# Optimization experiments

Hardware: AMD Instinct MI355X
Metric: run time of the kernel (lower is better)

The kernel has to match this reference:

```python
import jax, jax.numpy as jnp
import numpy as np

ALPHA = 1.5      # entmax alpha (q parameter)
N_ITER = 50      # entmax-bisect iterations (entmax library default)
B, S, DM, H, HKV, HD = 1, 2048, 2048, 16, 4, 128
ROPE_THETA = 10000.0


def _entmax_p(x):
    """alpha-entmax along last axis via bisection on tau (matches entmax.EntmaxBisect)."""
    am1 = ALPHA - 1.0
    pw = 1.0 / am1
    X = x * am1
    d = x.shape[-1]
    max_val = jnp.max(X, axis=-1, keepdims=True)
    tau_lo = max_val - 1.0                      # _gp(1, alpha) = 1
    tau_hi = max_val - (1.0 / d) ** am1          # _gp(1/d, alpha)
    dm0 = tau_hi - tau_lo

    def body(i, carry):
        tau_lo, dm, tau_m = carry
        dm = dm * 0.5
        tau_m = tau_lo + dm
        p = jnp.maximum(X - tau_m, 0.0) ** pw
        f = jnp.sum(p, axis=-1, keepdims=True) - 1.0
        tau_lo = jnp.where(f >= 0, tau_m, tau_lo)
        return (tau_lo, dm, tau_m)

    tau_lo, dm, tau_m = jax.lax.fori_loop(0, N_ITER, body, (tau_lo, dm0, tau_lo))
    p = jnp.maximum(X - tau_m, 0.0) ** pw
    return p / jnp.sum(p, axis=-1, keepdims=True)  # ensure_sum_one


@jax.custom_vjp
def entmax_bisect(x):
    return _entmax_p(x)

def _emx_fwd(x):
    p = _entmax_p(x)
    return p, p

def _emx_bwd(p, g):
    # entmax library backward: gppr = p^(2-alpha) on support
    gppr = jnp.where(p > 0, p ** (2.0 - ALPHA), 0.0)
    dX = g * gppr
    q = jnp.sum(dX, axis=-1, keepdims=True) / jnp.sum(gppr, axis=-1, keepdims=True)
    return ((dX - q * gppr),)

entmax_bisect.defvjp(_emx_fwd, _emx_bwd)


def _rotate_half(x):
    x1, x2 = x[..., : HD // 2], x[..., HD // 2:]
    return jnp.concatenate([-x2, x1], axis=-1)


def setup_inputs() -> dict:
    key = jax.random.key(0)
    k1, k2, k3, k4, k5 = jax.random.split(key, 5)
    hidden_states = jax.random.normal(k1, (B, S, DM), dtype=jnp.float32)
    wq = jax.random.normal(k2, (H * HD, DM), dtype=jnp.float32) * 0.02
    wk = jax.random.normal(k3, (HKV * HD, DM), dtype=jnp.float32) * 0.02
    wv = jax.random.normal(k4, (HKV * HD, DM), dtype=jnp.float32) * 0.02
    wo = jax.random.normal(k5, (DM, H * HD), dtype=jnp.float32) * 0.02
    # real Llama RoPE position embeddings
    inv_freq = 1.0 / (ROPE_THETA ** (np.arange(0, HD, 2, dtype=np.float32) / HD))
    pos = np.arange(S, dtype=np.float32)
    freqs = pos[:, None] * inv_freq[None, :]          # [S, HD/2]
    emb = np.concatenate([freqs, freqs], axis=-1)     # [S, HD]
    cos = jnp.asarray(np.cos(emb))[None]              # [1, S, HD]
    sin = jnp.asarray(np.sin(emb))[None]
    return {"hidden_states": hidden_states, "cos": cos, "sin": sin,
            "wq": wq, "wk": wk, "wv": wv, "wo": wo}


def reference(hidden_states, cos, sin, wq, wk, wv, wo):
    b, s, _ = hidden_states.shape
    scaling = HD ** -0.5
    # QKV projections -> [B, H, S, HD]
    q = (hidden_states @ wq.T).reshape(b, s, H, HD).transpose(0, 2, 1, 3)
    k = (hidden_states @ wk.T).reshape(b, s, HKV, HD).transpose(0, 2, 1, 3)
    v = (hidden_states @ wv.T).reshape(b, s, HKV, HD).transpose(0, 2, 1, 3)
    # RoPE (cos/sin broadcast over head axis)
    c, sn = cos[:, None, :, :], sin[:, None, :, :]
    q = q * c + _rotate_half(q) * sn
    k = k * c + _rotate_half(k) * sn
    # GQA: repeat kv heads
    g = H // HKV
    k = jnp.repeat(k, g, axis=1)
    v = jnp.repeat(v, g, axis=1)
    scores = jnp.einsum('bhqd,bhkd->bhqk', q, k) * scaling
    causal = jnp.tril(jnp.ones((s, s), dtype=bool))
    scores = jnp.where(causal, scores, -jnp.inf)
    attn = entmax_bisect(scores)                      # [B, H, S, S]
    out = jnp.einsum('bhqk,bhkd->bhqd', attn, v)
    out = out.transpose(0, 2, 1, 3).reshape(b, s, H * HD)
    out = out @ wo.T
    return (out, attn)
```

## Files before the change

### kernel.cpp

```cpp
#include <hip/hip_runtime.h>

typedef __bf16 bf16;
typedef __bf16 bf16x4 __attribute__((ext_vector_type(4)));
typedef __bf16 bf16x8 __attribute__((ext_vector_type(8)));
typedef float f32x4 __attribute__((ext_vector_type(4)));

#define S 2048
#define DM 2048
#define HD 128
#define H 16
#define NQKV 3072
#define NEWTON_ITERS 12

__device__ __forceinline__ void gl2lds16(const void* g, void* l) {
    __builtin_amdgcn_global_load_lds(
        (const __attribute__((address_space(1))) void*)g,
        (__attribute__((address_space(3))) void*)l, 16, 0, 0);
}

__device__ __forceinline__ void nt_store4(f32x4 v, float* p) {
    __builtin_nontemporal_store(v, (f32x4*)p);
}

__global__ void cvt_all(const float* __restrict__ hid, const float* __restrict__ wq,
                        const float* __restrict__ wk, const float* __restrict__ wv,
                        const float* __restrict__ wo, bf16* __restrict__ bh,
                        bf16* __restrict__ bqkv, bf16* __restrict__ bwo) {
    int i = blockIdx.x * blockDim.x + threadIdx.x;
    const float* src;
    bf16* dst;
    int off;
    if (i < 1048576) { src = hid; dst = bh; off = i; }
    else if (i < 2097152) { src = wq; dst = bqkv; off = i - 1048576; }
    else if (i < 2359296) { src = wk; dst = bqkv + 2048 * 2048; off = i - 2097152; }
    else if (i < 2621440) { src = wv; dst = bqkv + 2048 * 2048 + 512 * 2048; off = i - 2359296; }
    else { src = wo; dst = bwo; off = i - 2621440; }
    float4 f = ((const float4*)src)[off];
    bf16x4 o;
    o[0] = (bf16)f.x; o[1] = (bf16)f.y; o[2] = (bf16)f.z; o[3] = (bf16)f.w;
    ((bf16x4*)dst)[off] = o;
}

__global__ __launch_bounds__(256) void gemm128_bt(const bf16* __restrict__ A,
                                                  const bf16* __restrict__ B,
                                                  float* __restrict__ C, int Ndim, int K) {
    __shared__ bf16 As[128 * 32];
    __shared__ bf16 Bs[128 * 32];
    int m0 = blockIdx.x * 128, n0 = blockIdx.y * 128;
    int t = threadIdx.x;
    int l = t & 63, w = t >> 6;
    int lane16 = l & 15, quad = l >> 4;

    int c0 = (w * 2) * 64 + l;
    int c1 = c0 + 64;
    const bf16* Abase = A + (size_t)m0 * K;
    const bf16* Bbase = B + (size_t)n0 * K;

    int wm = (w & 1) * 64, wn = (w >> 1) * 64;
    f32x4 acc[4][4];
#pragma unroll
    for (int i = 0; i < 4; i++)
#pragma unroll
        for (int j = 0; j < 4; j++) acc[i][j] = (f32x4){0.f, 0.f, 0.f, 0.f};

    for (int k0 = 0; k0 < K; k0 += 32) {
        gl2lds16(Abase + (size_t)(c0 >> 2) * K + k0 + (c0 & 3) * 8, &As[(w * 2) * 512]);
        gl2lds16(Abase + (size_t)(c1 >> 2) * K + k0 + (c1 & 3) * 8, &As[(w * 2 + 1) * 512]);
        gl2lds16(Bbase + (size_t)(c0 >> 2) * K + k0 + (c0 & 3) * 8, &Bs[(w * 2) * 512]);
        gl2lds16(Bbase + (size_t)(c1 >> 2) * K + k0 + (c1 & 3) * 8, &Bs[(w * 2 + 1) * 512]);
        __syncthreads();
        bf16x8 af[4], bfr[4];
#pragma unroll
        for (int i = 0; i < 4; i++)
            af[i] = *(const bf16x8*)&As[(wm + i * 16 + lane16) * 32 + quad * 8];
#pragma unroll
        for (int j = 0; j < 4; j++)
            bfr[j] = *(const bf16x8*)&Bs[(wn + j * 16 + lane16) * 32 + quad * 8];
#pragma unroll
        for (int i = 0; i < 4; i++)
#pragma unroll
            for (int j = 0; j < 4; j++)
                acc[i][j] = __builtin_amdgcn_mfma_f32_16x16x32_bf16(af[i], bfr[j], acc[i][j], 0, 0, 0);
        __syncthreads();
    }
#pragma unroll
    for (int i = 0; i < 4; i++)
#pragma unroll
        for (int j = 0; j < 4; j++) {
            float* cp = C + (size_t)(m0 + wm + i * 16 + quad * 4) * Ndim + n0 + wn + j * 16 + lane16;
#pragma unroll
            for (int r = 0; r < 4; r++) cp[(size_t)r * Ndim] = acc[i][j][r];
        }
}

__global__ void rope_qk(const float* __restrict__ qkv, const float* __restrict__ cosb,
                        const float* __restrict__ sinb, bf16* __restrict__ qs,
                        bf16* __restrict__ kb) {
    int col = blockIdx.x * 256 + threadIdx.x;
    int s = blockIdx.y;
    const float* row = qkv + (size_t)s * NQKV;
    float v = row[col];
    if (col < DM) {
        int h = col >> 7, d = col & 127;
        float c = cosb[s * HD + d], sn = sinb[s * HD + d];
        float other = row[(h << 7) + ((d < 64) ? (d + 64) : (d - 64))];
        float rot = (d < 64) ? -other : other;
        float o = v * c + rot * sn;
        qs[((size_t)h * S + s) * HD + d] = (bf16)(o * 0.04419417382415922f);
    } else {
        int c2 = col - DM;
        int kv = c2 >> 7, d = c2 & 127;
        float c = cosb[s * HD + d], sn = sinb[s * HD + d];
        float other = row[DM + (kv << 7) + ((d < 64) ? (d + 64) : (d - 64))];
        float rot = (d < 64) ? -other : other;
        float o = v * c + rot * sn;
        kb[((size_t)kv * S + s) * HD + d] = (bf16)o;
    }
}

__global__ __launch_bounds__(256) void vtrans(const float* __restrict__ qkv, bf16* __restrict__ vT) {
    __shared__ bf16 tile[64][66];
    int s0 = blockIdx.x * 64, y0 = blockIdx.y * 64;
    int t = threadIdx.x;
    int ty = t & 63, tr = t >> 6;
#pragma unroll
    for (int i = 0; i < 16; i++) {
        int s = tr + i * 4;
        float v = qkv[(size_t)(s0 + s) * NQKV + 2560 + y0 + ty];
        tile[s][ty] = (bf16)v;
    }
    __syncthreads();
#pragma unroll
    for (int i = 0; i < 16; i++) {
        int y = tr + i * 4;
        vT[(size_t)(y0 + y) * S + s0 + ty] = tile[ty][y];
    }
}

template <int SEGS>
__device__ __forceinline__ void attn_body(const bf16* __restrict__ qs, const bf16* __restrict__ kb,
                                          const bf16* __restrict__ vT, float* __restrict__ attn,
                                          bf16* __restrict__ o, int r0, int h,
                                          float (&buf)[2][16][532]) {
    constexpr int NREG = SEGS * 8;
    int jlen = r0 + 16;
    int l = threadIdx.x & 63;
    int w = threadIdx.x >> 6;
    int lane16 = l & 15, quad = l >> 4;

    const bf16* qrow = qs + ((size_t)h * S + (r0 + lane16)) * HD + quad * 8;
    bf16x8 afrag[4];
#pragma unroll
    for (int kc = 0; kc < 4; kc++) afrag[kc] = *(const bf16x8*)(qrow + kc * 32);

    const bf16* kbase = kb + (size_t)(h >> 2) * S * HD;
    const bf16* vbase = vT + (size_t)(h >> 2) * HD * S;
    float xr[NREG];

#pragma unroll
    for (int sgi = 0; sgi < SEGS; sgi++) {
        int j0 = sgi * 512;
        float (*sb)[532] = buf[sgi & 1];
#pragma unroll
        for (int tt = 0; tt < 2; tt++) {
            int t = w + tt * 16;
            int jt = j0 + t * 16;
            if (jt < jlen) {
                f32x4 acc = {0.f, 0.f, 0.f, 0.f};
                const bf16* kp = kbase + (size_t)(jt + lane16) * HD + quad * 8;
#pragma unroll
                for (int kc = 0; kc < 4; kc++) {
                    bf16x8 b = *(const bf16x8*)(kp + kc * 32);
                    acc = __builtin_amdgcn_mfma_f32_16x16x32_bf16(afrag[kc], b, acc, 0, 0, 0);
                }
                if (jt + 15 > r0) {
                    int jj = jt + lane16;
#pragma unroll
                    for (int r = 0; r < 4; r++) {
                        int rowi = quad * 4 + r;
                        float v = acc[r];
                        if (jj > r0 + rowi) v = -1e30f;
                        sb[rowi][t * 16 + lane16] = v;
                    }
                } else {
#pragma unroll
                    for (int r = 0; r < 4; r++) sb[quad * 4 + r][t * 16 + lane16] = acc[r];
                }
            }
        }
        __syncthreads();
        if (sgi == SEGS - 1) {
#pragma unroll
            for (int part = 0; part < 2; part++) {
                float4 f = *(const float4*)&sb[w][part * 256 + l * 4];
                int jb = j0 + part * 256 + l * 4;
                xr[sgi * 8 + part * 4 + 0] = (jb + 0 < jlen) ? f.x : -1e30f;
                xr[sgi * 8 + part * 4 + 1] = (jb + 1 < jlen) ? f.y : -1e30f;
                xr[sgi * 8 + part * 4 + 2] = (jb + 2 < jlen) ? f.z : -1e30f;
                xr[sgi * 8 + part * 4 + 3] = (jb + 3 < jlen) ? f.w : -1e30f;
            }
        } else {
#pragma unroll
            for (int part = 0; part < 2; part++) {
                float4 f = *(const float4*)&sb[w][part * 256 + l * 4];
                xr[sgi * 8 + part * 4 + 0] = f.x;
                xr[sgi * 8 + part * 4 + 1] = f.y;
                xr[sgi * 8 + part * 4 + 2] = f.z;
                xr[sgi * 8 + part * 4 + 3] = f.w;
            }
        }
    }

    float m = -1e30f;
#pragma unroll
    for (int c = 0; c < NREG; c++) m = fmaxf(m, xr[c]);
#pragma unroll
    for (int off = 1; off < 64; off <<= 1) m = fmaxf(m, __shfl_xor(m, off));

    float tau = m - 1.0f;
#pragma unroll 1
    for (int it = 0; it < NEWTON_ITERS; it++) {
        float f0 = 0.f, f1 = 0.f, f2 = 0.f, f3 = 0.f;
        float g0 = 0.f, g1 = 0.f, g2 = 0.f, g3 = 0.f;
#pragma unroll
        for (int c = 0; c < NREG; c += 4) {
            float t0 = fmaxf(xr[c + 0] - tau, 0.f); f0 = fmaf(t0, t0, f0); g0 += t0;
            float t1 = fmaxf(xr[c + 1] - tau, 0.f); f1 = fmaf(t1, t1, f1); g1 += t1;
            float t2 = fmaxf(xr[c + 2] - tau, 0.f); f2 = fmaf(t2, t2, f2); g2 += t2;
            float t3 = fmaxf(xr[c + 3] - tau, 0.f); f3 = fmaf(t3, t3, f3); g3 += t3;
        }
        float f = (f0 + f1) + (f2 + f3);
        float g = (g0 + g1) + (g2 + g3);
#pragma unroll
        for (int off = 1; off < 64; off <<= 1) {
            f += __shfl_xor(f, off);
            g += __shfl_xor(g, off);
        }
        tau += (f - 1.0f) / (2.0f * g + 1e-20f);
    }

    float s0 = 0.f, s1 = 0.f, s2 = 0.f, s3 = 0.f;
#pragma unroll
    for (int c = 0; c < NREG; c += 4) {
        float t0 = fmaxf(xr[c + 0] - tau, 0.f); s0 = fmaf(t0, t0, s0);
        float t1 = fmaxf(xr[c + 1] - tau, 0.f); s1 = fmaf(t1, t1, s1);
        float t2 = fmaxf(xr[c + 2] - tau, 0.f); s2 = fmaf(t2, t2, s2);
        float t3 = fmaxf(xr[c + 3] - tau, 0.f); s3 = fmaf(t3, t3, s3);
    }
    float ssum = (s0 + s1) + (s2 + s3);
#pragma unroll
    for (int off = 1; off < 64; off <<= 1) ssum += __shfl_xor(ssum, off);
    float inv = 1.0f / ssum;

    int jt_o = (w & 7) * 16;
    int kh = (w >> 3) * 256;
    f32x4 acc_o = {0.f, 0.f, 0.f, 0.f};

    __syncthreads();
#pragma unroll
    for (int sgi = 0; sgi < SEGS; sgi++) {
        int j0 = sgi * 512;
        bf16 (*pbf)[552] = (bf16(*)[552])(&buf[sgi & 1][0][0]);
#pragma unroll
        for (int part = 0; part < 2; part++) {
            float t0 = fmaxf(xr[sgi * 8 + part * 4 + 0] - tau, 0.f);
            float t1 = fmaxf(xr[sgi * 8 + part * 4 + 1] - tau, 0.f);
            float t2 = fmaxf(xr[sgi * 8 + part * 4 + 2] - tau, 0.f);
            float t3 = fmaxf(xr[sgi * 8 + part * 4 + 3] - tau, 0.f);
            bf16x4 pbv;
            pbv[0] = (bf16)(t0 * t0 * inv); pbv[1] = (bf16)(t1 * t1 * inv);
            pbv[2] = (bf16)(t2 * t2 * inv); pbv[3] = (bf16)(t3 * t3 * inv);
            *(bf16x4*)&pbf[w][part * 256 + l * 4] = pbv;
        }
        __syncthreads();
#pragma unroll
        for (int ks = 0; ks < 8; ks++) {
            int kk = kh + ks * 32;
            bf16x8 a = *(const bf16x8*)&pbf[lane16][kk + quad * 8];
            bf16x8 b = *(const bf16x8*)(vbase + (size_t)(jt_o + lane16) * S + j0 + kk + quad * 8);
            acc_o = __builtin_amdgcn_mfma_f32_16x16x32_bf16(a, b, acc_o, 0, 0, 0);
        }
    }

    __syncthreads();
    if (w >= 8) {
#pragma unroll
        for (int r = 0; r < 4; r++) buf[0][w - 8][l * 4 + r] = acc_o[r];
    }
    __syncthreads();
    if (w < 8) {
        bf16* op = o + (size_t)(r0 + quad * 4) * DM + h * HD + jt_o + lane16;
#pragma unroll
        for (int r = 0; r < 4; r++) {
            float v = acc_o[r] + buf[0][w][l * 4 + r];
            op[(size_t)r * DM] = (bf16)v;
        }
    }

    float* arow = attn + ((size_t)h * S + (r0 + w)) * S;
#pragma unroll
    for (int sgi = 0; sgi < SEGS; sgi++) {
        int j0 = sgi * 512;
#pragma unroll
        for (int part = 0; part < 2; part++) {
            float t0 = fmaxf(xr[sgi * 8 + part * 4 + 0] - tau, 0.f);
            float t1 = fmaxf(xr[sgi * 8 + part * 4 + 1] - tau, 0.f);
            float t2 = fmaxf(xr[sgi * 8 + part * 4 + 2] - tau, 0.f);
            float t3 = fmaxf(xr[sgi * 8 + part * 4 + 3] - tau, 0.f);
            f32x4 pv;
            pv[0] = t0 * t0 * inv; pv[1] = t1 * t1 * inv;
            pv[2] = t2 * t2 * inv; pv[3] = t3 * t3 * inv;
            nt_store4(pv, &arow[j0 + part * 256 + l * 4]);
        }
    }
    f32x4 z4 = {0.f, 0.f, 0.f, 0.f};
    for (int j = SEGS * 512 + l * 4; j < S; j += 256) nt_store4(z4, &arow[j]);
}

__global__ __launch_bounds__(1024) void attn_av_all(const bf16* __restrict__ qs,
                                                    const bf16* __restrict__ kb,
                                                    const bf16* __restrict__ vT,
                                                    float* __restrict__ attn,
                                                    bf16* __restrict__ o) {
    __shared__ float buf[2][16][532];
    int b = blockIdx.x;
    int h = b & 15;
    int qh = b >> 4;
    attn_body<4>(qs, kb, vT, attn, o, (96 + qh) * 16, h, buf);
    __syncthreads();
    attn_body<3>(qs, kb, vT, attn, o, (64 + qh) * 16, h, buf);
    __syncthreads();
    attn_body<2>(qs, kb, vT, attn, o, (32 + qh) * 16, h, buf);
    __syncthreads();
    attn_body<1>(qs, kb, vT, attn, o, qh * 16, h, buf);
}

extern "C" void kernel_launch(void* const* d_in, const int* in_sizes, int n_in,
                              void* d_out, int out_size, void* d_ws, size_t ws_size,
                              hipStream_t stream) {
    const float* hidden = (const float*)d_in[0];
    const float* cosb   = (const float*)d_in[1];
    const float* sinb   = (const float*)d_in[2];
    const float* wq     = (const float*)d_in[3];
    const float* wk     = (const float*)d_in[4];
    const float* wv     = (const float*)d_in[5];
    const float* wo     = (const float*)d_in[6];
    char* ws = (char*)d_ws;
    bf16*  bf_hidden = (bf16*)(ws);
    bf16*  bf_wqkv   = (bf16*)(ws + 8388608);
    bf16*  bf_wo     = (bf16*)(ws + 20971520);
    float* qkv_raw   = (float*)(ws + 29360128);
    bf16*  qsb       = (bf16*)(ws + 54525952);
    bf16*  kbb       = (bf16*)(ws + 62914560);
    bf16*  vTb       = (bf16*)(ws + 65011712);
    float* out  = (float*)d_out;
    float* attn = out + 4194304;

    cvt_all<<<dim3(14336), 256, 0, stream>>>(hidden, wq, wk, wv, wo, bf_hidden, bf_wqkv, bf_wo);

    gemm128_bt<<<dim3(16, 24), 256, 0, stream>>>(bf_hidden, bf_wqkv, qkv_raw, NQKV, DM);

    rope_qk<<<dim3(10, S), 256, 0, stream>>>(qkv_raw, cosb, sinb, qsb, kbb);
    vtrans<<<dim3(32, 8), 256, 0, stream>>>(qkv_raw, vTb);

    attn_av_all<<<dim3(512), 1024, 0, stream>>>(qsb, kbb, vTb, attn, bf_hidden);

    gemm128_bt<<<dim3(16, 16), 256, 0, stream>>>(bf_hidden, bf_wo, out, DM, DM);
}
```

Measured before the change: 646.7 us.

## Use DPP wave reductions, packed f32x2 math, fused attn store, smaller GEMM tiles

Replaces the shuffle-based wave reductions in the entmax Newton loop with DPP row operations plus a readlane broadcast, and stores the scores as f32x2 so the compiler can emit packed FP32 math. The final attention-probability store is fused into the P·V loop, so the probabilities are not recomputed in a separate pass. Both projection GEMMs are templated and launched with 64x128 tiles, doubling the block count for more CU occupancy at the cost of less reuse per tile. The DPP reduction depends on row_bcast semantics, which is a correctness risk on newer architectures.

```diff
diff --git a/kernel.cpp b/kernel.cpp
--- a/kernel.cpp
+++ b/kernel.cpp
@@ -4,6 +4,7 @@
 typedef __bf16 bf16x4 __attribute__((ext_vector_type(4)));
 typedef __bf16 bf16x8 __attribute__((ext_vector_type(8)));
 typedef float f32x4 __attribute__((ext_vector_type(4)));
+typedef float f32x2 __attribute__((ext_vector_type(2)));
 
 #define S 2048
 #define DM 2048
@@ -20,6 +21,38 @@
 
 __device__ __forceinline__ void nt_store4(f32x4 v, float* p) {
     __builtin_nontemporal_store(v, (f32x4*)p);
+}
+
+template <int CTRL, int RM>
+__device__ __forceinline__ float dpp_zero(float x) {
+    return __builtin_bit_cast(float, __builtin_amdgcn_update_dpp(
+        0, __builtin_bit_cast(int, x), CTRL, RM, 0xf, false));
+}
+template <int CTRL, int RM>
+__device__ __forceinline__ float dpp_self(float x) {
+    int xi = __builtin_bit_cast(int, x);
+    return __builtin_bit_cast(float, __builtin_amdgcn_update_dpp(xi, xi, CTRL, RM, 0xf, false));
+}
+__device__ __forceinline__ float wave_bcast63(float x) {
+    return __builtin_bit_cast(float, __builtin_amdgcn_readlane(__builtin_bit_cast(int, x), 63));
+}
+__device__ __forceinline__ float wave_sum(float x) {
+    x += dpp_zero<0x111, 0xf>(x);
+    x += dpp_zero<0x112, 0xf>(x);
+    x += dpp_zero<0x114, 0xf>(x);
+    x += dpp_zero<0x118, 0xf>(x);
+    x += dpp_zero<0x142, 0xa>(x);
+    x += dpp_zero<0x143, 0xc>(x);
+    return wave_bcast63(x);
+}
+__device__ __forceinline__ float wave_fmax(float x) {
+    x = fmaxf(x, dpp_self<0x111, 0xf>(x));
+    x = fmaxf(x, dpp_self<0x112, 0xf>(x));
+    x = fmaxf(x, dpp_self<0x114, 0xf>(x));
+    x = fmaxf(x, dpp_self<0x118, 0xf>(x));
+    x = fmaxf(x, dpp_self<0x142, 0xa>(x));
+    x = fmaxf(x, dpp_self<0x143, 0xc>(x));
+    return wave_bcast63(x);
 }
 
 __global__ void cvt_all(const float* __restrict__ hid, const float* __restrict__ wq,
@@ -41,52 +74,61 @@
     ((bf16x4*)dst)[off] = o;
 }
 
-__global__ __launch_bounds__(256) void gemm128_bt(const bf16* __restrict__ A,
-                                                  const bf16* __restrict__ B,
-                                                  float* __restrict__ C, int Ndim, int K) {
-    __shared__ bf16 As[128 * 32];
-    __shared__ bf16 Bs[128 * 32];
-    int m0 = blockIdx.x * 128, n0 = blockIdx.y * 128;
+template <int BM, int BN>
+__global__ __launch_bounds__(256) void gemm_bt(const bf16* __restrict__ A,
+                                               const bf16* __restrict__ B,
+                                               float* __restrict__ C, int Ndim, int K) {
+    __shared__ bf16 As[BM * 32];
+    __shared__ bf16 Bs[BN * 32];
+    int m0 = blockIdx.x * BM, n0 = blockIdx.y * BN;
     int t = threadIdx.x;
     int l = t & 63, w = t >> 6;
     int lane16 = l & 15, quad = l >> 4;
 
-    int c0 = (w * 2) * 64 + l;
-    int c1 = c0 + 64;
     const bf16* Abase = A + (size_t)m0 * K;
     const bf16* Bbase = B + (size_t)n0 * K;
 
-    int wm = (w & 1) * 64, wn = (w >> 1) * 64;
-    f32x4 acc[4][4];
-#pragma unroll
-    for (int i = 0; i < 4; i++)
-#pragma unroll
-        for (int j = 0; j < 4; j++) acc[i][j] = (f32x4){0.f, 0.f, 0.f, 0.f};
+    constexpr int MI = BM / 32, NI = BN / 32;
+    int wm = (w & 1) * (BM / 2), wn = (w >> 1) * (BN / 2);
+    f32x4 acc[MI][NI];
+#pragma unroll
+    for (int i = 0; i < MI; i++)
+#pragma unroll
+        for (int j = 0; j < NI; j++) acc[i][j] = (f32x4){0.f, 0.f, 0.f, 0.f};
+
+    constexpr int AG = BM * 4;
+    constexpr int BG = BN * 4;
 
     for (int k0 = 0; k0 < K; k0 += 32) {
-        gl2lds16(Abase + (size_t)(c0 >> 2) * K + k0 + (c0 & 3) * 8, &As[(w * 2) * 512]);
-        gl2lds16(Abase + (size_t)(c1 >> 2) * K + k0 + (c1 & 3) * 8, &As[(w * 2 + 1) * 512]);
-        gl2lds16(Bbase + (size_t)(c0 >> 2) * K + k0 + (c0 & 3) * 8, &Bs[(w * 2) * 512]);
-        gl2lds16(Bbase + (size_t)(c1 >> 2) * K + k0 + (c1 & 3) * 8, &Bs[(w * 2 + 1) * 512]);
+#pragma unroll
+        for (int it = 0; it < AG / 256; it++) {
+            int c = it * 256 + t;
+            gl2lds16(Abase + (size_t)(c >> 2) * K + k0 + (c & 3) * 8, &As[(c - l) * 8]);
+        }
+#pragma unroll
+        for (int it = 0; it < BG / 256; it++) {
+            int c = it * 256 + t;
+            gl2lds16(Bbase + (size_t)(c >> 2) * K + k0 + (c & 3) * 8, &Bs[(c - l) * 8]);
+        }
         __syncthreads();
-        bf16x8 af[4], bfr[4];
-#pragma unroll
-        for (int i = 0; i < 4; i++)
+        bf16x8 af[MI], bfr[NI];
+#pragma unroll
+        for (int i = 0; i < MI; i++)
             af[i] = *(const bf16x8*)&As[(wm + i * 16 + lane16) * 32 + quad * 8];
 #pragma unroll
-        for (int j = 0; j < 4; j++)
+        for (int j = 0; j < NI; j++)
             bfr[j] = *(const bf16x8*)&Bs[(wn + j * 16 + lane16) * 32 + quad * 8];
 #pragma unroll
-        for (int i = 0; i < 4; i++)
-#pragma unroll
-            for (int j = 0; j < 4; j++)
+        for (int i = 0; i < MI; i++)
+#pragma unroll
+            for (int j = 0; j < NI; j++)
                 acc[i][j] = __builtin_amdgcn_mfma_f32_16x16x32_bf16(af[i], bfr[j], acc[i][j], 0, 0, 0);
         __syncthreads();
     }
 #pragma unroll
-    for (int i = 0; i < 4; i++)
-#pragma unroll
-        for (int j = 0; j < 4; j++) {
+    for (int i = 0; i < MI; i++)
+#pragma unroll
+        for (int j = 0; j < NI; j++) {
             float* cp = C + (size_t)(m0 + wm + i * 16 + quad * 4) * Ndim + n0 + wn + j * 16 + lane16;
 #pragma unroll
             for (int r = 0; r < 4; r++) cp[(size_t)r * Ndim] = acc[i][j][r];
@@ -142,7 +184,7 @@
                                           const bf16* __restrict__ vT, float* __restrict__ attn,
                                           bf16* __restrict__ o, int r0, int h,
                                           float (&buf)[2][16][532]) {
-    constexpr int NREG = SEGS * 8;
+    constexpr int NREG2 = SEGS * 4;
     int jlen = r0 + 16;
     int l = threadIdx.x & 63;
     int w = threadIdx.x >> 6;
@@ -155,7 +197,7 @@
 
     const bf16* kbase = kb + (size_t)(h >> 2) * S * HD;
     const bf16* vbase = vT + (size_t)(h >> 2) * HD * S;
-    float xr[NREG];
+    f32x2 xr[NREG2];
 
 #pragma unroll
     for (int sgi = 0; sgi < SEGS; sgi++) {
@@ -189,72 +231,67 @@
             }
         }
         __syncthreads();
-        if (sgi == SEGS - 1) {
-#pragma unroll
-            for (int part = 0; part < 2; part++) {
-                float4 f = *(const float4*)&sb[w][part * 256 + l * 4];
+#pragma unroll
+        for (int part = 0; part < 2; part++) {
+            float4 fq = *(const float4*)&sb[w][part * 256 + l * 4];
+            if (sgi == SEGS - 1) {
                 int jb = j0 + part * 256 + l * 4;
-                xr[sgi * 8 + part * 4 + 0] = (jb + 0 < jlen) ? f.x : -1e30f;
-                xr[sgi * 8 + part * 4 + 1] = (jb + 1 < jlen) ? f.y : -1e30f;
-                xr[sgi * 8 + part * 4 + 2] = (jb + 2 < jlen) ? f.z : -1e30f;
-                xr[sgi * 8 + part * 4 + 3] = (jb + 3 < jlen) ? f.w : -1e30f;
+                xr[sgi * 4 + part * 2 + 0] =
+                    (f32x2){(jb + 0 < jlen) ? fq.x : -1e30f, (jb + 1 < jlen) ? fq.y : -1e30f};
+                xr[sgi * 4 + part * 2 + 1] =
+                    (f32x2){(jb + 2 < jlen) ? fq.z : -1e30f, (jb + 3 < jlen) ? fq.w : -1e30f};
+            } else {
+                xr[sgi * 4 + part * 2 + 0] = (f32x2){fq.x, fq.y};
+                xr[sgi * 4 + part * 2 + 1] = (f32x2){fq.z, fq.w};
             }
-        } else {
-#pragma unroll
-            for (int part = 0; part < 2; part++) {
-                float4 f = *(const float4*)&sb[w][part * 256 + l * 4];
-                xr[sgi * 8 + part * 4 + 0] = f.x;
-                xr[sgi * 8 + part * 4 + 1] = f.y;
-                xr[sgi * 8 + part * 4 + 2] = f.z;
-                xr[sgi * 8 + part * 4 + 3] = f.w;
-            }
-        }
-    }
-
-    float m = -1e30f;
-#pragma unroll
-    for (int c = 0; c < NREG; c++) m = fmaxf(m, xr[c]);
-#pragma unroll
-    for (int off = 1; off < 64; off <<= 1) m = fmaxf(m, __shfl_xor(m, off));
+        }
+    }
+
+    const f32x2 z2 = {0.f, 0.f};
+    float mx = -1e30f;
+#pragma unroll
+    for (int c = 0; c < NREG2; c++) mx = fmaxf(mx, fmaxf(xr[c][0], xr[c][1]));
+    float m = wave_fmax(mx);
 
     float tau = m - 1.0f;
 #pragma unroll 1
     for (int it = 0; it < NEWTON_ITERS; it++) {
-        float f0 = 0.f, f1 = 0.f, f2 = 0.f, f3 = 0.f;
-        float g0 = 0.f, g1 = 0.f, g2 = 0.f, g3 = 0.f;
-#pragma unroll
-        for (int c = 0; c < NREG; c += 4) {
-            float t0 = fmaxf(xr[c + 0] - tau, 0.f); f0 = fmaf(t0, t0, f0); g0 += t0;
-            float t1 = fmaxf(xr[c + 1] - tau, 0.f); f1 = fmaf(t1, t1, f1); g1 += t1;
-            float t2 = fmaxf(xr[c + 2] - tau, 0.f); f2 = fmaf(t2, t2, f2); g2 += t2;
-            float t3 = fmaxf(xr[c + 3] - tau, 0.f); f3 = fmaf(t3, t3, f3); g3 += t3;
-        }
-        float f = (f0 + f1) + (f2 + f3);
-        float g = (g0 + g1) + (g2 + g3);
-#pragma unroll
-        for (int off = 1; off < 64; off <<= 1) {
-            f += __shfl_xor(f, off);
-            g += __shfl_xor(g, off);
-        }
+        f32x2 tvi = {tau, tau};
+        f32x2 fa = z2, fb = z2, ga = z2, gb = z2;
+#pragma unroll
+        for (int c = 0; c < NREG2; c += 2) {
+            f32x2 t0 = __builtin_elementwise_max(xr[c] - tvi, z2);
+            fa += t0 * t0; ga += t0;
+            f32x2 t1 = __builtin_elementwise_max(xr[c + 1] - tvi, z2);
+            fb += t1 * t1; gb += t1;
+        }
+        f32x2 fv = fa + fb, gv = ga + gb;
+        float f = wave_sum(fv[0] + fv[1]);
+        float g = wave_sum(gv[0] + gv[1]);
         tau += (f - 1.0f) / (2.0f * g + 1e-20f);
     }
 
-    float s0 = 0.f, s1 = 0.f, s2 = 0.f, s3 = 0.f;
-#pragma unroll
-    for (int c = 0; c < NREG; c += 4) {
-        float t0 = fmaxf(xr[c + 0] - tau, 0.f); s0 = fmaf(t0, t0, s0);
-        float t1 = fmaxf(xr[c + 1] - tau, 0.f); s1 = fmaf(t1, t1, s1);
-        float t2 = fmaxf(xr[c + 2] - tau, 0.f); s2 = fmaf(t2, t2, s2);
-        float t3 = fmaxf(xr[c + 3] - tau, 0.f); s3 = fmaf(t3, t3, s3);
-    }
-    float ssum = (s0 + s1) + (s2 + s3);
-#pragma unroll
-    for (int off = 1; off < 64; off <<= 1) ssum += __shfl_xor(ssum, off);
-    float inv = 1.0f / ssum;
+    f32x2 tv = {tau, tau};
+    float inv;
+    {
+        f32x2 sa = z2, sbv = z2;
+#pragma unroll
+        for (int c = 0; c < NREG2; c += 2) {
+            f32x2 t0 = __builtin_elementwise_max(xr[c] - tv, z2);
+            sa += t0 * t0;
+            f32x2 t1 = __builtin_elementwise_max(xr[c + 1] - tv, z2);
+            sbv += t1 * t1;
+        }
+        f32x2 sv = sa + sbv;
+        float ssum = wave_sum(sv[0] + sv[1]);
+        inv = 1.0f / ssum;
+    }
 
     int jt_o = (w & 7) * 16;
     int kh = (w >> 3) * 256;
     f32x4 acc_o = {0.f, 0.f, 0.f, 0.f};
+    float* arow = attn + ((size_t)h * S + (r0 + w)) * S;
+    f32x2 inv2 = {inv, inv};
 
     __syncthreads();
 #pragma unroll
@@ -263,13 +300,15 @@
         bf16 (*pbf)[552] = (bf16(*)[552])(&buf[sgi & 1][0][0]);
 #pragma unroll
         for (int part = 0; part < 2; part++) {
-            float t0 = fmaxf(xr[sgi * 8 + part * 4 + 0] - tau, 0.f);
-            float t1 = fmaxf(xr[sgi * 8 + part * 4 + 1] - tau, 0.f);
-            float t2 = fmaxf(xr[sgi * 8 + part * 4 + 2] - tau, 0.f);
-            float t3 = fmaxf(xr[sgi * 8 + part * 4 + 3] - tau, 0.f);
+            f32x2 ta = __builtin_elementwise_max(xr[sgi * 4 + part * 2 + 0] - tv, z2);
+            f32x2 tb = __builtin_elementwise_max(xr[sgi * 4 + part * 2 + 1] - tv, z2);
+            f32x2 pa = (ta * ta) * inv2;
+            f32x2 pb = (tb * tb) * inv2;
+            f32x4 pv = {pa[0], pa[1], pb[0], pb[1]};
+            nt_store4(pv, &arow[j0 + part * 256 + l * 4]);
             bf16x4 pbv;
-            pbv[0] = (bf16)(t0 * t0 * inv); pbv[1] = (bf16)(t1 * t1 * inv);
-            pbv[2] = (bf16)(t2 * t2 * inv); pbv[3] = (bf16)(t3 * t3 * inv);
+            pbv[0] = (bf16)pv[0]; pbv[1] = (bf16)pv[1];
+            pbv[2] = (bf16)pv[2]; pbv[3] = (bf16)pv[3];
             *(bf16x4*)&pbf[w][part * 256 + l * 4] = pbv;
         }
         __syncthreads();
@@ -297,22 +336,6 @@
         }
     }
 
-    float* arow = attn + ((size_t)h * S + (r0 + w)) * S;
-#pragma unroll
-    for (int sgi = 0; sgi < SEGS; sgi++) {
-        int j0 = sgi * 512;
-#pragma unroll
-        for (int part = 0; part < 2; part++) {
-            float t0 = fmaxf(xr[sgi * 8 + part * 4 + 0] - tau, 0.f);
-            float t1 = fmaxf(xr[sgi * 8 + part * 4 + 1] - tau, 0.f);
-            float t2 = fmaxf(xr[sgi * 8 + part * 4 + 2] - tau, 0.f);
-            float t3 = fmaxf(xr[sgi * 8 + part * 4 + 3] - tau, 0.f);
-            f32x4 pv;
-            pv[0] = t0 * t0 * inv; pv[1] = t1 * t1 * inv;
-            pv[2] = t2 * t2 * inv; pv[3] = t3 * t3 * inv;
-            nt_store4(pv, &arow[j0 + part * 256 + l * 4]);
-        }
-    }
     f32x4 z4 = {0.f, 0.f, 0.f, 0.f};
     for (int j = SEGS * 512 + l * 4; j < S; j += 256) nt_store4(z4, &arow[j]);
 }
@@ -358,12 +381,12 @@
 
     cvt_all<<<dim3(14336), 256, 0, stream>>>(hidden, wq, wk, wv, wo, bf_hidden, bf_wqkv, bf_wo);
 
-    gemm128_bt<<<dim3(16, 24), 256, 0, stream>>>(bf_hidden, bf_wqkv, qkv_raw, NQKV, DM);
+    gemm_bt<64, 128><<<dim3(32, 24), 256, 0, stream>>>(bf_hidden, bf_wqkv, qkv_raw, NQKV, DM);
 
     rope_qk<<<dim3(10, S), 256, 0, stream>>>(qkv_raw, cosb, sinb, qsb, kbb);
     vtrans<<<dim3(32, 8), 256, 0, stream>>>(qkv_raw, vTb);
 
     attn_av_all<<<dim3(512), 1024, 0, stream>>>(qsb, kbb, vTb, attn, bf_hidden);
 
-    gemm128_bt<<<dim3(16, 16), 256, 0, stream>>>(bf_hidden, bf_wo, out, DM, DM);
-}
+    gemm_bt<64, 128><<<dim3(32, 16), 256, 0, stream>>>(bf_hidden, bf_wo, out, DM, DM);
+}
```

After: 618.2 us. -4.4%, faster.
